# Performance work log

Hardware: AMD Instinct MI355X
Metric: run time of the kernel (lower is better)

## Reference

```python
import jax, jax.numpy as jnp
import numpy as np

N_EDGES = 320000
N_PARTICLES = 10000
EMBED = 256
N_RBF = 16
OUT_EMBED = 512


def setup_inputs() -> dict:
    key = jax.random.key(0)
    ks = jax.random.split(key, 9)
    s = 0.05
    return {
        "messages": jax.random.normal(ks[0], (N_EDGES, EMBED), dtype=jnp.float32),
        "rbf": jax.random.normal(ks[1], (N_EDGES, N_RBF), dtype=jnp.float32),
        "idx_i": jax.random.randint(ks[2], (N_EDGES,), 0, N_PARTICLES, dtype=jnp.int32),
        "W_rbf": jax.random.normal(ks[3], (N_RBF, EMBED), dtype=jnp.float32) * s,
        "W_up": jax.random.normal(ks[4], (EMBED, OUT_EMBED), dtype=jnp.float32) * s,
        "W_d0": jax.random.normal(ks[5], (OUT_EMBED, OUT_EMBED), dtype=jnp.float32) * s,
        "b_d0": jnp.zeros((OUT_EMBED,), dtype=jnp.float32),
        "W_d1": jax.random.normal(ks[6], (OUT_EMBED, OUT_EMBED), dtype=jnp.float32) * s,
        "b_d1": jnp.zeros((OUT_EMBED,), dtype=jnp.float32),
        "W_final": jax.random.normal(ks[7], (OUT_EMBED, 1), dtype=jnp.float32) * s,
    }


def reference(messages, rbf, idx_i, W_rbf, W_up, W_d0, b_d0, W_d1, b_d1, W_final):
    # rbf_dense: [n_edges, n_rbf] @ [n_rbf, embed] -> gate per edge
    transformed_rbf = rbf @ W_rbf
    gated = messages * transformed_rbf                      # [n_edges, embed]
    # high-precision scatter-add over receiver atoms (fp32 accumulation)
    summed = jax.ops.segment_sum(gated, idx_i, num_segments=N_PARTICLES)
    up = summed @ W_up                                      # [n_particles, out_embed]
    up = jax.nn.swish(up @ W_d0 + b_d0)
    up = jax.nn.swish(up @ W_d1 + b_d1)
    per_atom_targets = up @ W_final                         # [n_particles, 1]
    return per_atom_targets
```

## Files before the change

kernel.cpp:

```cpp
#include <hip/hip_runtime.h>
#include <hip/hip_bf16.h>
#include <math.h>

#define N_EDGES_C 320000
#define N_PART 10000
#define EMBED 256
#define NRBF 16
#define OUTE 512

typedef __attribute__((ext_vector_type(8))) short short8;
typedef __attribute__((ext_vector_type(4))) float float4v;

#define WS_SUMMED   0
#define WS_BUF0     6000000
#define WS_BUF1     17000000
#define WS_WTUP     28000000
#define WS_WTD0     28300000
#define WS_WTD1     28900000
#define WS_CNT      29500000
#define WS_CUR      29540000
#define WS_OFF      29580000
#define WS_ELIST    29640000

__global__ __launch_bounds__(256) void hist_kernel(
    const int* __restrict__ idx_i, int* __restrict__ cnt)
{
    int e = blockIdx.x * 256 + threadIdx.x;
    if (e < N_EDGES_C) atomicAdd(&cnt[idx_i[e]], 1);
}

__global__ __launch_bounds__(256) void scan_kernel(
    const int* __restrict__ cnt, int* __restrict__ off)
{
    __shared__ int s[256];
    const int t = threadIdx.x;
    const int base = t * 40;
    int v[40];
    int loc = 0;
#pragma unroll
    for (int i = 0; i < 40; ++i) {
        int idx = base + i;
        int c = (idx < N_PART) ? cnt[idx] : 0;
        v[i] = c;
        loc += c;
    }
    s[t] = loc;
    __syncthreads();
    for (int d = 1; d < 256; d <<= 1) {
        int x = (t >= d) ? s[t - d] : 0;
        __syncthreads();
        s[t] += x;
        __syncthreads();
    }
    int pre = (t > 0) ? s[t - 1] : 0;
#pragma unroll
    for (int i = 0; i < 40; ++i) {
        int idx = base + i;
        if (idx < N_PART) off[idx] = pre;
        pre += v[i];
    }
}

__global__ __launch_bounds__(256) void fill_kernel(
    const int* __restrict__ idx_i, const int* __restrict__ off,
    int* __restrict__ cur, int* __restrict__ elist)
{
    int e = blockIdx.x * 256 + threadIdx.x;
    if (e >= N_EDGES_C) return;
    int p = idx_i[e];
    int pos = atomicAdd(&cur[p], 1);
    elist[off[p] + pos] = e;
}

__global__ __launch_bounds__(256) void gather_kernel(
    const float* __restrict__ messages, const float* __restrict__ rbf,
    const float* __restrict__ W_rbf, const int* __restrict__ off,
    const int* __restrict__ cnt, const int* __restrict__ elist,
    __hip_bfloat16* __restrict__ summed)
{
    __shared__ float w[NRBF][EMBED];
    const int c = threadIdx.x;
    const int p = blockIdx.x;
#pragma unroll
    for (int k = 0; k < NRBF; ++k) w[k][c] = W_rbf[k * EMBED + c];
    __syncthreads();

    const int base = off[p];
    const int deg  = cnt[p];
    float acc = 0.f;
    for (int j = 0; j < deg; ++j) {
        const int e = elist[base + j];
        const float4* r4 = (const float4*)(rbf + (size_t)e * NRBF);
        float4 r0 = r4[0], r1 = r4[1], r2 = r4[2], r3 = r4[3];
        float t = 0.f;
        t = fmaf(r0.x, w[0][c], t);  t = fmaf(r0.y, w[1][c], t);
        t = fmaf(r0.z, w[2][c], t);  t = fmaf(r0.w, w[3][c], t);
        t = fmaf(r1.x, w[4][c], t);  t = fmaf(r1.y, w[5][c], t);
        t = fmaf(r1.z, w[6][c], t);  t = fmaf(r1.w, w[7][c], t);
        t = fmaf(r2.x, w[8][c], t);  t = fmaf(r2.y, w[9][c], t);
        t = fmaf(r2.z, w[10][c], t); t = fmaf(r2.w, w[11][c], t);
        t = fmaf(r3.x, w[12][c], t); t = fmaf(r3.y, w[13][c], t);
        t = fmaf(r3.z, w[14][c], t); t = fmaf(r3.w, w[15][c], t);
        acc = fmaf(messages[(size_t)e * EMBED + c], t, acc);
    }
    summed[(size_t)p * EMBED + c] = __float2bfloat16(acc);
}

__global__ __launch_bounds__(256) void transpose_cvt(
    const float* __restrict__ W, __hip_bfloat16* __restrict__ Wt, int K, int N)
{
    __shared__ float t[32][33];
    const int bn = blockIdx.x * 32;
    const int bk = blockIdx.y * 32;
    const int x = threadIdx.x & 31;
    const int y8 = threadIdx.x >> 5;
#pragma unroll
    for (int yy = y8; yy < 32; yy += 8)
        t[yy][x] = W[(size_t)(bk + yy) * N + bn + x];
    __syncthreads();
#pragma unroll
    for (int yy = y8; yy < 32; yy += 8)
        Wt[(size_t)(bn + yy) * K + bk + x] = __float2bfloat16(t[x][yy]);
}

#define BM 128
#define BN 128
#define BK 32
#define LDSP 40

template <int ACT>
__global__ __launch_bounds__(256) void gemm_mfma(
    const __hip_bfloat16* __restrict__ A,
    const __hip_bfloat16* __restrict__ Bt,
    const float* __restrict__ bias,
    __hip_bfloat16* __restrict__ C,
    int M, int K, int N)
{
    __shared__ short As[BM * LDSP];
    __shared__ short Bs[BN * LDSP];

    const int tid  = threadIdx.x;
    const int bm   = blockIdx.x * BM;
    const int bn   = blockIdx.y * BN;
    const int wave = tid >> 6;
    const int lane = tid & 63;
    const int wm   = (wave >> 1) * 64;
    const int wn   = (wave & 1) * 64;
    const int l16  = lane & 15;
    const int quad = lane >> 4;

    float4v acc[4][4];
#pragma unroll
    for (int i = 0; i < 4; ++i)
#pragma unroll
        for (int j = 0; j < 4; ++j)
#pragma unroll
            for (int r = 0; r < 4; ++r) acc[i][j][r] = 0.f;

    const int sr = tid >> 1;
    const int sh = (tid & 1) * 16;

    for (int k0 = 0; k0 < K; k0 += BK) {
        short8 av0, av1;
        if (bm + sr < M) {
            const short8* ga = (const short8*)((const short*)A + (size_t)(bm + sr) * K + k0 + sh);
            av0 = ga[0];
            av1 = ga[1];
        } else {
#pragma unroll
            for (int i = 0; i < 8; ++i) { av0[i] = 0; av1[i] = 0; }
        }
        *(short8*)&As[sr * LDSP + sh]     = av0;
        *(short8*)&As[sr * LDSP + sh + 8] = av1;
        const short8* gb = (const short8*)((const short*)Bt + (size_t)(bn + sr) * K + k0 + sh);
        short8 bv0 = gb[0], bv1 = gb[1];
        *(short8*)&Bs[sr * LDSP + sh]     = bv0;
        *(short8*)&Bs[sr * LDSP + sh + 8] = bv1;
        __syncthreads();

        short8 af[4], bf[4];
#pragma unroll
        for (int mt = 0; mt < 4; ++mt)
            af[mt] = *(const short8*)&As[(wm + mt * 16 + l16) * LDSP + quad * 8];
#pragma unroll
        for (int nt = 0; nt < 4; ++nt)
            bf[nt] = *(const short8*)&Bs[(wn + nt * 16 + l16) * LDSP + quad * 8];
#pragma unroll
        for (int mt = 0; mt < 4; ++mt)
#pragma unroll
            for (int nt = 0; nt < 4; ++nt)
                acc[mt][nt] = __builtin_amdgcn_mfma_f32_16x16x32_bf16(
                    af[mt], bf[nt], acc[mt][nt], 0, 0, 0);
        __syncthreads();
    }

#pragma unroll
    for (int mt = 0; mt < 4; ++mt) {
        const int row0 = bm + wm + mt * 16 + quad * 4;
#pragma unroll
        for (int nt = 0; nt < 4; ++nt) {
            const int col = bn + wn + nt * 16 + l16;
            const float bv = bias ? bias[col] : 0.f;
#pragma unroll
            for (int r = 0; r < 4; ++r) {
                const int rr = row0 + r;
                if (rr < M) {
                    float v = acc[mt][nt][r] + bv;
                    if (ACT == 1) v = v / (1.f + expf(-v));
                    C[(size_t)rr * N + col] = __float2bfloat16(v);
                }
            }
        }
    }
}

__global__ __launch_bounds__(256) void final_dot(
    const __hip_bfloat16* __restrict__ up, const float* __restrict__ Wf,
    float* __restrict__ out)
{
    const int wave = threadIdx.x >> 6;
    const int lane = threadIdx.x & 63;
    const int p = blockIdx.x * 4 + wave;
    if (p >= N_PART) return;
    float s = 0.f;
#pragma unroll
    for (int k = lane; k < OUTE; k += 64)
        s = fmaf(__bfloat162float(up[(size_t)p * OUTE + k]), Wf[k], s);
#pragma unroll
    for (int off = 32; off > 0; off >>= 1) s += __shfl_down(s, off);
    if (lane == 0) out[p] = s;
}

extern "C" void kernel_launch(void* const* d_in, const int* in_sizes, int n_in,
                              void* d_out, int out_size, void* d_ws, size_t ws_size,
                              hipStream_t stream) {
    const float* messages = (const float*)d_in[0];
    const float* rbf      = (const float*)d_in[1];
    const int*   idx_i    = (const int*)d_in[2];
    const float* W_rbf    = (const float*)d_in[3];
    const float* W_up     = (const float*)d_in[4];
    const float* W_d0     = (const float*)d_in[5];
    const float* b_d0     = (const float*)d_in[6];
    const float* W_d1     = (const float*)d_in[7];
    const float* b_d1     = (const float*)d_in[8];
    const float* W_final  = (const float*)d_in[9];
    float* out = (float*)d_out;

    char* ws = (char*)d_ws;
    __hip_bfloat16* summed = (__hip_bfloat16*)(ws + WS_SUMMED);
    __hip_bfloat16* buf0   = (__hip_bfloat16*)(ws + WS_BUF0);
    __hip_bfloat16* buf1   = (__hip_bfloat16*)(ws + WS_BUF1);
    __hip_bfloat16* wt_up  = (__hip_bfloat16*)(ws + WS_WTUP);
    __hip_bfloat16* wt_d0  = (__hip_bfloat16*)(ws + WS_WTD0);
    __hip_bfloat16* wt_d1  = (__hip_bfloat16*)(ws + WS_WTD1);
    int* cnt   = (int*)(ws + WS_CNT);
    int* cur   = (int*)(ws + WS_CUR);
    int* offp  = (int*)(ws + WS_OFF);
    int* elist = (int*)(ws + WS_ELIST);

    hipMemsetAsync(ws + WS_CNT, 0, 80000, stream);

    hist_kernel<<<(N_EDGES_C + 255) / 256, 256, 0, stream>>>(idx_i, cnt);
    scan_kernel<<<1, 256, 0, stream>>>(cnt, offp);
    fill_kernel<<<(N_EDGES_C + 255) / 256, 256, 0, stream>>>(idx_i, offp, cur, elist);

    transpose_cvt<<<dim3(OUTE / 32, EMBED / 32), 256, 0, stream>>>(W_up,  wt_up,  EMBED, OUTE);
    transpose_cvt<<<dim3(OUTE / 32, OUTE  / 32), 256, 0, stream>>>(W_d0,  wt_d0,  OUTE,  OUTE);
    transpose_cvt<<<dim3(OUTE / 32, OUTE  / 32), 256, 0, stream>>>(W_d1,  wt_d1,  OUTE,  OUTE);

    gather_kernel<<<N_PART, 256, 0, stream>>>(messages, rbf, W_rbf, offp, cnt,
                                              elist, summed);

    dim3 g((N_PART + BM - 1) / BM, OUTE / BN);
    gemm_mfma<0><<<g, 256, 0, stream>>>(summed, wt_up, nullptr, buf0,
                                        N_PART, EMBED, OUTE);
    gemm_mfma<1><<<g, 256, 0, stream>>>(buf0, wt_d0, b_d0, buf1,
                                        N_PART, OUTE, OUTE);
    gemm_mfma<1><<<g, 256, 0, stream>>>(buf1, wt_d1, b_d1, buf0,
                                        N_PART, OUTE, OUTE);

    final_dot<<<(N_PART + 3) / 4, 256, 0, stream>>>(buf0, W_final, out);
}
```

Before: 673.0 us.

## Stage edge lists in LDS, unroll gather, fuse final dot, merge transposes

The gather kernel now loads each node's edge indices into shared memory in chunks and unrolls the accumulation by four, so more independent message and rbf loads are in flight. The final W_final dot product is fused into the last GEMM epilogue using shuffle reductions and atomicAdd into a zeroed output, which avoids writing and rereading the last activation buffer. The three weight transposes are merged into one launch, and the scan uses 1024 threads. The cost is extra atomics and an output memset, and the summation order becomes nondeterministic.

```diff
diff --git a/kernel.cpp b/kernel.cpp
--- a/kernel.cpp
+++ b/kernel.cpp
@@ -29,16 +29,16 @@
     if (e < N_EDGES_C) atomicAdd(&cnt[idx_i[e]], 1);
 }
 
-__global__ __launch_bounds__(256) void scan_kernel(
+__global__ __launch_bounds__(1024) void scan_kernel(
     const int* __restrict__ cnt, int* __restrict__ off)
 {
-    __shared__ int s[256];
+    __shared__ int s[1024];
     const int t = threadIdx.x;
-    const int base = t * 40;
-    int v[40];
+    const int base = t * 10;
+    int v[10];
     int loc = 0;
 #pragma unroll
-    for (int i = 0; i < 40; ++i) {
+    for (int i = 0; i < 10; ++i) {
         int idx = base + i;
         int c = (idx < N_PART) ? cnt[idx] : 0;
         v[i] = c;
@@ -46,7 +46,7 @@
     }
     s[t] = loc;
     __syncthreads();
-    for (int d = 1; d < 256; d <<= 1) {
+    for (int d = 1; d < 1024; d <<= 1) {
         int x = (t >= d) ? s[t - d] : 0;
         __syncthreads();
         s[t] += x;
@@ -54,7 +54,7 @@
     }
     int pre = (t > 0) ? s[t - 1] : 0;
 #pragma unroll
-    for (int i = 0; i < 40; ++i) {
+    for (int i = 0; i < 10; ++i) {
         int idx = base + i;
         if (idx < N_PART) off[idx] = pre;
         pre += v[i];
@@ -72,6 +72,23 @@
     elist[off[p] + pos] = e;
 }
 
+__device__ __forceinline__ float rbf_gate(
+    const float* __restrict__ rbf, int e, const float (*w)[EMBED], int c)
+{
+    const float4* r4 = (const float4*)(rbf + (size_t)e * NRBF);
+    float4 r0 = r4[0], r1 = r4[1], r2 = r4[2], r3 = r4[3];
+    float t = 0.f;
+    t = fmaf(r0.x, w[0][c], t);  t = fmaf(r0.y, w[1][c], t);
+    t = fmaf(r0.z, w[2][c], t);  t = fmaf(r0.w, w[3][c], t);
+    t = fmaf(r1.x, w[4][c], t);  t = fmaf(r1.y, w[5][c], t);
+    t = fmaf(r1.z, w[6][c], t);  t = fmaf(r1.w, w[7][c], t);
+    t = fmaf(r2.x, w[8][c], t);  t = fmaf(r2.y, w[9][c], t);
+    t = fmaf(r2.z, w[10][c], t); t = fmaf(r2.w, w[11][c], t);
+    t = fmaf(r3.x, w[12][c], t); t = fmaf(r3.y, w[13][c], t);
+    t = fmaf(r3.z, w[14][c], t); t = fmaf(r3.w, w[15][c], t);
+    return t;
+}
+
 __global__ __launch_bounds__(256) void gather_kernel(
     const float* __restrict__ messages, const float* __restrict__ rbf,
     const float* __restrict__ W_rbf, const int* __restrict__ off,
@@ -79,36 +96,59 @@
     __hip_bfloat16* __restrict__ summed)
 {
     __shared__ float w[NRBF][EMBED];
+    __shared__ int el[256];
     const int c = threadIdx.x;
     const int p = blockIdx.x;
 #pragma unroll
     for (int k = 0; k < NRBF; ++k) w[k][c] = W_rbf[k * EMBED + c];
-    __syncthreads();
 
     const int base = off[p];
     const int deg  = cnt[p];
     float acc = 0.f;
-    for (int j = 0; j < deg; ++j) {
-        const int e = elist[base + j];
-        const float4* r4 = (const float4*)(rbf + (size_t)e * NRBF);
-        float4 r0 = r4[0], r1 = r4[1], r2 = r4[2], r3 = r4[3];
-        float t = 0.f;
-        t = fmaf(r0.x, w[0][c], t);  t = fmaf(r0.y, w[1][c], t);
-        t = fmaf(r0.z, w[2][c], t);  t = fmaf(r0.w, w[3][c], t);
-        t = fmaf(r1.x, w[4][c], t);  t = fmaf(r1.y, w[5][c], t);
-        t = fmaf(r1.z, w[6][c], t);  t = fmaf(r1.w, w[7][c], t);
-        t = fmaf(r2.x, w[8][c], t);  t = fmaf(r2.y, w[9][c], t);
-        t = fmaf(r2.z, w[10][c], t); t = fmaf(r2.w, w[11][c], t);
-        t = fmaf(r3.x, w[12][c], t); t = fmaf(r3.y, w[13][c], t);
-        t = fmaf(r3.z, w[14][c], t); t = fmaf(r3.w, w[15][c], t);
-        acc = fmaf(messages[(size_t)e * EMBED + c], t, acc);
+
+    for (int ch = 0; ch < deg; ch += 256) {
+        const int n = min(256, deg - ch);
+        if (c < n) el[c] = elist[base + ch + c];
+        __syncthreads();
+
+        int j = 0;
+        for (; j + 4 <= n; j += 4) {
+            const int e0 = el[j], e1 = el[j + 1], e2 = el[j + 2], e3 = el[j + 3];
+            const float m0 = messages[(size_t)e0 * EMBED + c];
+            const float m1 = messages[(size_t)e1 * EMBED + c];
+            const float m2 = messages[(size_t)e2 * EMBED + c];
+            const float m3 = messages[(size_t)e3 * EMBED + c];
+            const float t0 = rbf_gate(rbf, e0, w, c);
+            const float t1 = rbf_gate(rbf, e1, w, c);
+            const float t2 = rbf_gate(rbf, e2, w, c);
+            const float t3 = rbf_gate(rbf, e3, w, c);
+            acc = fmaf(m0, t0, acc);
+            acc = fmaf(m1, t1, acc);
+            acc = fmaf(m2, t2, acc);
+            acc = fmaf(m3, t3, acc);
+        }
+        for (; j < n; ++j) {
+            const int e = el[j];
+            const float m = messages[(size_t)e * EMBED + c];
+            acc = fmaf(m, rbf_gate(rbf, e, w, c), acc);
+        }
+        __syncthreads();
     }
     summed[(size_t)p * EMBED + c] = __float2bfloat16(acc);
 }
 
-__global__ __launch_bounds__(256) void transpose_cvt(
-    const float* __restrict__ W, __hip_bfloat16* __restrict__ Wt, int K, int N)
-{
+__global__ __launch_bounds__(256) void transpose_cvt_all(
+    const float* __restrict__ W_up, const float* __restrict__ W_d0,
+    const float* __restrict__ W_d1, __hip_bfloat16* __restrict__ wt_up,
+    __hip_bfloat16* __restrict__ wt_d0, __hip_bfloat16* __restrict__ wt_d1)
+{
+    const int z = blockIdx.z;
+    const float* W = (z == 0) ? W_up : (z == 1) ? W_d0 : W_d1;
+    __hip_bfloat16* Wt = (z == 0) ? wt_up : (z == 1) ? wt_d0 : wt_d1;
+    const int K = (z == 0) ? EMBED : OUTE;
+    const int N = OUTE;
+    if (blockIdx.y * 32 >= K) return;
+
     __shared__ float t[32][33];
     const int bn = blockIdx.x * 32;
     const int bk = blockIdx.y * 32;
@@ -128,12 +168,14 @@
 #define BK 32
 #define LDSP 40
 
-template <int ACT>
+template <int ACT, int FUSE>
 __global__ __launch_bounds__(256) void gemm_mfma(
     const __hip_bfloat16* __restrict__ A,
     const __hip_bfloat16* __restrict__ Bt,
     const float* __restrict__ bias,
     __hip_bfloat16* __restrict__ C,
+    const float* __restrict__ Wf,
+    float* __restrict__ out,
     int M, int K, int N)
 {
     __shared__ short As[BM * LDSP];
@@ -194,41 +236,51 @@
         __syncthreads();
     }
 
-#pragma unroll
-    for (int mt = 0; mt < 4; ++mt) {
-        const int row0 = bm + wm + mt * 16 + quad * 4;
+    if (!FUSE) {
+#pragma unroll
+        for (int mt = 0; mt < 4; ++mt) {
+            const int row0 = bm + wm + mt * 16 + quad * 4;
+#pragma unroll
+            for (int nt = 0; nt < 4; ++nt) {
+                const int col = bn + wn + nt * 16 + l16;
+                const float bv = bias ? bias[col] : 0.f;
+#pragma unroll
+                for (int r = 0; r < 4; ++r) {
+                    const int rr = row0 + r;
+                    if (rr < M) {
+                        float v = acc[mt][nt][r] + bv;
+                        if (ACT == 1) v = v / (1.f + expf(-v));
+                        C[(size_t)rr * N + col] = __float2bfloat16(v);
+                    }
+                }
+            }
+        }
+    } else {
+        float bv[4], wfv[4];
 #pragma unroll
         for (int nt = 0; nt < 4; ++nt) {
             const int col = bn + wn + nt * 16 + l16;
-            const float bv = bias ? bias[col] : 0.f;
+            bv[nt]  = bias ? bias[col] : 0.f;
+            wfv[nt] = Wf[col];
+        }
+#pragma unroll
+        for (int mt = 0; mt < 4; ++mt) {
 #pragma unroll
             for (int r = 0; r < 4; ++r) {
-                const int rr = row0 + r;
-                if (rr < M) {
-                    float v = acc[mt][nt][r] + bv;
+                const int row = bm + wm + mt * 16 + quad * 4 + r;
+                float s = 0.f;
+#pragma unroll
+                for (int nt = 0; nt < 4; ++nt) {
+                    float v = acc[mt][nt][r] + bv[nt];
                     if (ACT == 1) v = v / (1.f + expf(-v));
-                    C[(size_t)rr * N + col] = __float2bfloat16(v);
+                    s = fmaf(v, wfv[nt], s);
                 }
+#pragma unroll
+                for (int o = 8; o > 0; o >>= 1) s += __shfl_down(s, o);
+                if (l16 == 0 && row < M) atomicAdd(&out[row], s);
             }
         }
     }
-}
-
-__global__ __launch_bounds__(256) void final_dot(
-    const __hip_bfloat16* __restrict__ up, const float* __restrict__ Wf,
-    float* __restrict__ out)
-{
-    const int wave = threadIdx.x >> 6;
-    const int lane = threadIdx.x & 63;
-    const int p = blockIdx.x * 4 + wave;
-    if (p >= N_PART) return;
-    float s = 0.f;
-#pragma unroll
-    for (int k = lane; k < OUTE; k += 64)
-        s = fmaf(__bfloat162float(up[(size_t)p * OUTE + k]), Wf[k], s);
-#pragma unroll
-    for (int off = 32; off > 0; off >>= 1) s += __shfl_down(s, off);
-    if (lane == 0) out[p] = s;
 }
 
 extern "C" void kernel_launch(void* const* d_in, const int* in_sizes, int n_in,
@@ -259,25 +311,23 @@
     int* elist = (int*)(ws + WS_ELIST);
 
     hipMemsetAsync(ws + WS_CNT, 0, 80000, stream);
+    hipMemsetAsync(d_out, 0, (size_t)N_PART * sizeof(float), stream);
 
     hist_kernel<<<(N_EDGES_C + 255) / 256, 256, 0, stream>>>(idx_i, cnt);
-    scan_kernel<<<1, 256, 0, stream>>>(cnt, offp);
+    scan_kernel<<<1, 1024, 0, stream>>>(cnt, offp);
     fill_kernel<<<(N_EDGES_C + 255) / 256, 256, 0, stream>>>(idx_i, offp, cur, elist);
 
-    transpose_cvt<<<dim3(OUTE / 32, EMBED / 32), 256, 0, stream>>>(W_up,  wt_up,  EMBED, OUTE);
-    transpose_cvt<<<dim3(OUTE / 32, OUTE  / 32), 256, 0, stream>>>(W_d0,  wt_d0,  OUTE,  OUTE);
-    transpose_cvt<<<dim3(OUTE / 32, OUTE  / 32), 256, 0, stream>>>(W_d1,  wt_d1,  OUTE,  OUTE);
+    transpose_cvt_all<<<dim3(OUTE / 32, OUTE / 32, 3), 256, 0, stream>>>(
+        W_up, W_d0, W_d1, wt_up, wt_d0, wt_d1);
 
     gather_kernel<<<N_PART, 256, 0, stream>>>(messages, rbf, W_rbf, offp, cnt,
                                               elist, summed);
 
     dim3 g((N_PART + BM - 1) / BM, OUTE / BN);
-    gemm_mfma<0><<<g, 256, 0, stream>>>(summed, wt_up, nullptr, buf0,
-                                        N_PART, EMBED, OUTE);
-    gemm_mfma<1><<<g, 256, 0, stream>>>(buf0, wt_d0, b_d0, buf1,
-                                        N_PART, OUTE, OUTE);
-    gemm_mfma<1><<<g, 256, 0, stream>>>(buf1, wt_d1, b_d1, buf0,
-                                        N_PART, OUTE, OUTE);
-
-    final_dot<<<(N_PART + 3) / 4, 256, 0, stream>>>(buf0, W_final, out);
-}
+    gemm_mfma<0, 0><<<g, 256, 0, stream>>>(summed, wt_up, nullptr, buf0,
+                                           nullptr, nullptr, N_PART, EMBED, OUTE);
+    gemm_mfma<1, 0><<<g, 256, 0, stream>>>(buf0, wt_d0, b_d0, buf1,
+                                           nullptr, nullptr, N_PART, OUTE, OUTE);
+    gemm_mfma<1, 1><<<g, 256, 0, stream>>>(buf1, wt_d1, b_d1, nullptr,
+                                           W_final, out, N_PART, OUTE, OUTE);
+}
```

New measurement: 625.9 us. 1.08x faster.
